# Optimization experiments

Measured on AMD Instinct MI355X. Metric: run time of the kernel, lower is better.

## Reference

```python
import jax, jax.numpy as jnp
import numpy as np

HIDDEN = 768
NUM_LABELS = 64


def setup_inputs() -> dict:
    key = jax.random.key(0)
    k1, k2, k3, k4, k5 = jax.random.split(key, 5)
    B, S = 16, 4096
    com_features = jax.random.normal(k1, (B, S, HIDDEN), dtype=jnp.float32)
    labels = jax.random.randint(k2, (B, S), 0, NUM_LABELS + 1, dtype=jnp.int64)
    label_feature = jax.random.normal(k3, (NUM_LABELS, HIDDEN), dtype=jnp.float32)
    # nn.Linear(1536, 768): weight [out, in], bias [out]
    merge_w = jax.random.normal(k4, (HIDDEN, 2 * HIDDEN), dtype=jnp.float32) * (1.0 / np.sqrt(2 * HIDDEN))
    merge_b = jax.random.normal(k5, (HIDDEN,), dtype=jnp.float32) * 0.01
    return {"com_features": com_features, "labels": labels,
            "label_feature": label_feature, "merge_w": merge_w, "merge_b": merge_b}


def reference(com_features, labels, label_feature, merge_w, merge_b):
    B, S, H = com_features.shape
    tokens_emb = com_features.reshape(-1, H)          # [N, H]
    token_labels = labels.reshape(-1)                  # [N]
    active = token_labels != 0                         # label 0 = inactive
    # label_id = label - 1 indexes the concatenated label-feature table.
    # Clip so inactive rows gather a valid (ignored) row; result is masked out.
    label_id = jnp.clip(token_labels - 1, 0, label_feature.shape[0] - 1)
    centers = label_feature[label_id]                  # [N, H] gather
    # merge(cat(token_emb, center)) == token @ W_left^T + center @ W_right^T + b
    cat = jnp.concatenate([tokens_emb, centers], axis=-1)  # [N, 2H]
    merged = cat @ merge_w.T + merge_b                 # [N, H]
    # scatter_ back into token embeddings: active rows replaced by merged.
    out = jnp.where(active[:, None], merged, tokens_emb)
    return out.reshape(B, S, H)
```

## Files before the change

kernel.cpp:

```cpp
#include <hip/hip_runtime.h>
#include <hip/hip_bf16.h>

#define HID 768
#define WROW 1536
#define NLAB 64

typedef __attribute__((ext_vector_type(8))) __bf16 bf16x8;
typedef __attribute__((ext_vector_type(4))) float f32x4;

__device__ __forceinline__ void async16(const void* g, void* l) {
    __builtin_amdgcn_global_load_lds(
        (const __attribute__((address_space(1))) void*)g,
        (__attribute__((address_space(3))) void*)l,
        16, 0, 0);
}

__global__ __launch_bounds__(256) void compute_P_kernel(
    const float* __restrict__ lf,
    const float* __restrict__ W,
    const float* __restrict__ bias,
    float* __restrict__ P)
{
    const int l = blockIdx.x;
    const int t = threadIdx.x;
    __shared__ float lfs[HID];
    for (int i = t; i < HID; i += 256) lfs[i] = lf[l * HID + i];
    __syncthreads();

    #pragma unroll
    for (int jj = 0; jj < 3; ++jj) {
        const int j = jj * 256 + t;
        const float* wr = W + (size_t)j * WROW + HID;
        float acc = bias[j];
        for (int k = 0; k < HID; k += 4) {
            float4 u = *(const float4*)(wr + k);
            acc += lfs[k] * u.x + lfs[k + 1] * u.y
                 + lfs[k + 2] * u.z + lfs[k + 3] * u.w;
        }
        P[l * HID + j] = acc;
    }
}

__global__ __launch_bounds__(256) void merge_gemm_kernel(
    const float* __restrict__ A,
    const int* __restrict__ labels,
    const float* __restrict__ W,
    const float* __restrict__ P,
    float* __restrict__ out)
{
    __shared__ float As[128 * 32];
    __shared__ float Bs[128 * 32];
    __shared__ int Ls[128];

    const int t  = threadIdx.x;
    const int m0 = blockIdx.y * 128;
    const int j0 = blockIdx.x * 128;

    if (t < 128) Ls[t] = labels[m0 + t];

    const int w  = t >> 6;
    const int l  = t & 63;
    const int lm = l & 15;
    const int lk = l >> 4;
    const int qm = (w >> 1) * 64;
    const int qn = (w & 1) * 64;

    f32x4 acc[4][4] = {};

    const int sr = t >> 3;
    const int sc = ((t & 7) ^ (sr & 7)) * 4;
    const float* gA = A + (size_t)(m0 + sr) * HID + sc;
    const float* gB = W + (size_t)(j0 + sr) * WROW + sc;
    float* lA = As + t * 4;
    float* lB = Bs + t * 4;

    for (int k0 = 0; k0 < HID; k0 += 32) {
        #pragma unroll
        for (int i = 0; i < 4; ++i) {
            async16(gA + (size_t)(32 * i) * HID + k0, lA + 1024 * i);
            async16(gB + (size_t)(32 * i) * WROW + k0, lB + 1024 * i);
        }
        __syncthreads();

        bf16x8 af[4], bfr[4];
        #pragma unroll
        for (int mi = 0; mi < 4; ++mi) {
            const int r = qm + mi * 16 + lm;
            const int s = r & 7;
            f32x4 lo = *(const f32x4*)(As + r * 32 + ((2 * lk) ^ s) * 4);
            f32x4 hi = *(const f32x4*)(As + r * 32 + ((2 * lk + 1) ^ s) * 4);
            af[mi] = (bf16x8){(__bf16)lo.x, (__bf16)lo.y, (__bf16)lo.z, (__bf16)lo.w,
                              (__bf16)hi.x, (__bf16)hi.y, (__bf16)hi.z, (__bf16)hi.w};
        }
        #pragma unroll
        for (int ni = 0; ni < 4; ++ni) {
            const int r = qn + ni * 16 + lm;
            const int s = r & 7;
            f32x4 lo = *(const f32x4*)(Bs + r * 32 + ((2 * lk) ^ s) * 4);
            f32x4 hi = *(const f32x4*)(Bs + r * 32 + ((2 * lk + 1) ^ s) * 4);
            bfr[ni] = (bf16x8){(__bf16)lo.x, (__bf16)lo.y, (__bf16)lo.z, (__bf16)lo.w,
                               (__bf16)hi.x, (__bf16)hi.y, (__bf16)hi.z, (__bf16)hi.w};
        }

        #pragma unroll
        for (int mi = 0; mi < 4; ++mi)
            #pragma unroll
            for (int ni = 0; ni < 4; ++ni)
                acc[mi][ni] = __builtin_amdgcn_mfma_f32_16x16x32_bf16(
                    af[mi], bfr[ni], acc[mi][ni], 0, 0, 0);

        __syncthreads();
    }

    #pragma unroll
    for (int mi = 0; mi < 4; ++mi) {
        const int rowb = qm + mi * 16 + lk * 4;
        #pragma unroll
        for (int r = 0; r < 4; ++r) {
            const int n_tok = m0 + rowb + r;
            const int lab   = Ls[rowb + r];
            const size_t rowoff = (size_t)n_tok * HID;
            #pragma unroll
            for (int ni = 0; ni < 4; ++ni) {
                const int j = j0 + qn + ni * 16 + lm;
                float v;
                if (lab != 0)
                    v = acc[mi][ni][r] + P[(size_t)(lab - 1) * HID + j];
                else
                    v = A[rowoff + j];
                out[rowoff + j] = v;
            }
        }
    }
}

extern "C" void kernel_launch(void* const* d_in, const int* in_sizes, int n_in,
                              void* d_out, int out_size, void* d_ws, size_t ws_size,
                              hipStream_t stream) {
    const float* com    = (const float*)d_in[0];
    const int*   labels = (const int*)d_in[1];
    const float* lf     = (const float*)d_in[2];
    const float* W      = (const float*)d_in[3];
    const float* bias   = (const float*)d_in[4];
    float* out = (float*)d_out;
    float* P = (float*)d_ws;

    const int n_rows = in_sizes[0] / HID;
    compute_P_kernel<<<dim3(NLAB), dim3(256), 0, stream>>>(lf, W, bias, P);
    merge_gemm_kernel<<<dim3(HID / 128, n_rows / 128), dim3(256), 0, stream>>>(
        com, labels, W, P, out);
}
```

Before: 611.1 us.

## Register-prefetch bf16 LDS double buffering, XCD block remap, and parallel P kernel

The GEMM kernel drops the async global-to-LDS fp32 loads. It now loads fp32 into registers, converts to bf16 once, and stores into double-buffered bf16 LDS. The next tile's global loads are issued before the MFMA work, and one barrier per iteration is removed. Blocks are remapped with a 1D grid and an 8-way XCD-aware swizzle for cache locality, and the P precompute is parallelised to one block per output column with a shuffle reduction. This trades extra register pressure for less LDS traffic, less repeated conversion and better latency hiding.

Result: faster. 531.0 us (-13.1%).

```diff
diff --git a/kernel.cpp b/kernel.cpp
--- a/kernel.cpp
+++ b/kernel.cpp
@@ -8,11 +8,9 @@
 typedef __attribute__((ext_vector_type(8))) __bf16 bf16x8;
 typedef __attribute__((ext_vector_type(4))) float f32x4;
 
-__device__ __forceinline__ void async16(const void* g, void* l) {
-    __builtin_amdgcn_global_load_lds(
-        (const __attribute__((address_space(1))) void*)g,
-        (__attribute__((address_space(3))) void*)l,
-        16, 0, 0);
+__device__ __forceinline__ bf16x8 pk8(float4 a, float4 b) {
+    return (bf16x8){(__bf16)a.x, (__bf16)a.y, (__bf16)a.z, (__bf16)a.w,
+                    (__bf16)b.x, (__bf16)b.y, (__bf16)b.z, (__bf16)b.w};
 }
 
 __global__ __launch_bounds__(256) void compute_P_kernel(
@@ -21,24 +19,28 @@
     const float* __restrict__ bias,
     float* __restrict__ P)
 {
-    const int l = blockIdx.x;
+    const int j = blockIdx.x;
     const int t = threadIdx.x;
-    __shared__ float lfs[HID];
-    for (int i = t; i < HID; i += 256) lfs[i] = lf[l * HID + i];
+    __shared__ __align__(16) float wrow[HID];
+    if (t < 192)
+        *(float4*)(wrow + t * 4) =
+            *(const float4*)(W + (size_t)j * WROW + HID + t * 4);
     __syncthreads();
 
-    #pragma unroll
-    for (int jj = 0; jj < 3; ++jj) {
-        const int j = jj * 256 + t;
-        const float* wr = W + (size_t)j * WROW + HID;
-        float acc = bias[j];
-        for (int k = 0; k < HID; k += 4) {
-            float4 u = *(const float4*)(wr + k);
-            acc += lfs[k] * u.x + lfs[k + 1] * u.y
-                 + lfs[k + 2] * u.z + lfs[k + 3] * u.w;
-        }
-        P[l * HID + j] = acc;
+    const int lab = t >> 2;
+    const int seg = t & 3;
+    const float* lfp = lf + lab * HID + seg * 192;
+    const float* wp  = wrow + seg * 192;
+    float acc = 0.f;
+    #pragma unroll 8
+    for (int i = 0; i < 192; i += 4) {
+        float4 u = *(const float4*)(lfp + i);
+        float4 v = *(const float4*)(wp + i);
+        acc += u.x * v.x + u.y * v.y + u.z * v.z + u.w * v.w;
     }
+    acc += __shfl_xor(acc, 1);
+    acc += __shfl_xor(acc, 2);
+    if (seg == 0) P[lab * HID + j] = acc + bias[j];
 }
 
 __global__ __launch_bounds__(256) void merge_gemm_kernel(
@@ -46,16 +48,22 @@
     const int* __restrict__ labels,
     const float* __restrict__ W,
     const float* __restrict__ P,
-    float* __restrict__ out)
+    float* __restrict__ out,
+    const int nwg)
 {
-    __shared__ float As[128 * 32];
-    __shared__ float Bs[128 * 32];
+    __shared__ __align__(16) unsigned short As[2][128 * 32];
+    __shared__ __align__(16) unsigned short Bs[2][128 * 32];
     __shared__ int Ls[128];
 
-    const int t  = threadIdx.x;
-    const int m0 = blockIdx.y * 128;
-    const int j0 = blockIdx.x * 128;
+    int bid = blockIdx.x;
+    if ((nwg & 7) == 0) {
+        const int q = nwg >> 3;
+        bid = (bid & 7) * q + (bid >> 3);
+    }
+    const int m0 = (bid / (HID / 128)) * 128;
+    const int j0 = (bid % (HID / 128)) * 128;
 
+    const int t = threadIdx.x;
     if (t < 128) Ls[t] = labels[m0 + t];
 
     const int w  = t >> 6;
@@ -65,41 +73,44 @@
     const int qm = (w >> 1) * 64;
     const int qn = (w & 1) * 64;
 
+    const int sr = t >> 2;
+    const int sc = t & 3;
+    const float* gA  = A + (size_t)(m0 + sr) * HID  + sc * 8;
+    const float* gA2 = gA + (size_t)64 * HID;
+    const float* gB  = W + (size_t)(j0 + sr) * WROW + sc * 8;
+    const float* gB2 = gB + (size_t)64 * WROW;
+    const int eoff = sr * 32 + ((sc ^ (sr & 3)) * 8);
+
+    float4 ra0, ra1, ra2, ra3, rb0, rb1, rb2, rb3;
     f32x4 acc[4][4] = {};
 
-    const int sr = t >> 3;
-    const int sc = ((t & 7) ^ (sr & 7)) * 4;
-    const float* gA = A + (size_t)(m0 + sr) * HID + sc;
-    const float* gB = W + (size_t)(j0 + sr) * WROW + sc;
-    float* lA = As + t * 4;
-    float* lB = Bs + t * 4;
+#define ISSUE(K) do { \
+    ra0 = *(const float4*)(gA  + (K));      ra1 = *(const float4*)(gA  + (K) + 4); \
+    ra2 = *(const float4*)(gA2 + (K));      ra3 = *(const float4*)(gA2 + (K) + 4); \
+    rb0 = *(const float4*)(gB  + (K));      rb1 = *(const float4*)(gB  + (K) + 4); \
+    rb2 = *(const float4*)(gB2 + (K));      rb3 = *(const float4*)(gB2 + (K) + 4); \
+} while (0)
 
+    ISSUE(0);
+    int p = 0;
     for (int k0 = 0; k0 < HID; k0 += 32) {
-        #pragma unroll
-        for (int i = 0; i < 4; ++i) {
-            async16(gA + (size_t)(32 * i) * HID + k0, lA + 1024 * i);
-            async16(gB + (size_t)(32 * i) * WROW + k0, lB + 1024 * i);
-        }
+        *(bf16x8*)&As[p][eoff]        = pk8(ra0, ra1);
+        *(bf16x8*)&As[p][eoff + 2048] = pk8(ra2, ra3);
+        *(bf16x8*)&Bs[p][eoff]        = pk8(rb0, rb1);
+        *(bf16x8*)&Bs[p][eoff + 2048] = pk8(rb2, rb3);
+        if (k0 + 32 < HID) ISSUE(k0 + 32);
         __syncthreads();
 
         bf16x8 af[4], bfr[4];
         #pragma unroll
         for (int mi = 0; mi < 4; ++mi) {
             const int r = qm + mi * 16 + lm;
-            const int s = r & 7;
-            f32x4 lo = *(const f32x4*)(As + r * 32 + ((2 * lk) ^ s) * 4);
-            f32x4 hi = *(const f32x4*)(As + r * 32 + ((2 * lk + 1) ^ s) * 4);
-            af[mi] = (bf16x8){(__bf16)lo.x, (__bf16)lo.y, (__bf16)lo.z, (__bf16)lo.w,
-                              (__bf16)hi.x, (__bf16)hi.y, (__bf16)hi.z, (__bf16)hi.w};
+            af[mi] = *(const bf16x8*)&As[p][r * 32 + ((lk ^ (r & 3)) * 8)];
         }
         #pragma unroll
         for (int ni = 0; ni < 4; ++ni) {
             const int r = qn + ni * 16 + lm;
-            const int s = r & 7;
-            f32x4 lo = *(const f32x4*)(Bs + r * 32 + ((2 * lk) ^ s) * 4);
-            f32x4 hi = *(const f32x4*)(Bs + r * 32 + ((2 * lk + 1) ^ s) * 4);
-            bfr[ni] = (bf16x8){(__bf16)lo.x, (__bf16)lo.y, (__bf16)lo.z, (__bf16)lo.w,
-                               (__bf16)hi.x, (__bf16)hi.y, (__bf16)hi.z, (__bf16)hi.w};
+            bfr[ni] = *(const bf16x8*)&Bs[p][r * 32 + ((lk ^ (r & 3)) * 8)];
         }
 
         #pragma unroll
@@ -109,8 +120,9 @@
                 acc[mi][ni] = __builtin_amdgcn_mfma_f32_16x16x32_bf16(
                     af[mi], bfr[ni], acc[mi][ni], 0, 0, 0);
 
-        __syncthreads();
+        p ^= 1;
     }
+#undef ISSUE
 
     #pragma unroll
     for (int mi = 0; mi < 4; ++mi) {
@@ -146,7 +158,8 @@
     float* P = (float*)d_ws;
 
     const int n_rows = in_sizes[0] / HID;
-    compute_P_kernel<<<dim3(NLAB), dim3(256), 0, stream>>>(lf, W, bias, P);
-    merge_gemm_kernel<<<dim3(HID / 128, n_rows / 128), dim3(256), 0, stream>>>(
-        com, labels, W, P, out);
+    compute_P_kernel<<<dim3(HID), dim3(256), 0, stream>>>(lf, W, bias, P);
+    const int nwg = (n_rows / 128) * (HID / 128);
+    merge_gemm_kernel<<<dim3(nwg), dim3(256), 0, stream>>>(
+        com, labels, W, P, out, nwg);
 }
```
